# Kernel tuning notes

Hardware: AMD Instinct MI355X
Metric: run time of the kernel (lower is better)

The kernel has to match this reference:

```python
import jax, jax.numpy as jnp
import numpy as np

N_NODES = 50000
N_EDGES = 800000
D_FEAT = 64


def setup_inputs() -> dict:
    key = jax.random.key(0)
    k_h, k_src, k_dst = jax.random.split(key, 3)
    h = jax.random.normal(k_h, (N_NODES, D_FEAT), dtype=jnp.float32)
    src = jax.random.randint(k_src, (N_EDGES,), 0, N_NODES, dtype=jnp.int64)
    dst = jax.random.randint(k_dst, (N_EDGES,), 0, N_NODES, dtype=jnp.int64)
    return {"h": h, "src": src, "dst": dst}


def reference(h, src, dst):
    # DGL u_mul_v: per-edge elementwise product of source and destination node features.
    # z[e, :] = h[src[e], :] * h[dst[e], :]   -> shape [E, D]
    return h[src] * h[dst]
```

## Files before the change

kernel.cpp:

```cpp
#include <hip/hip_runtime.h>
#include <hip/hip_bf16.h>


#define D_FEAT 64
#define CHUNKS_PER_EDGE 16

__global__ __launch_bounds__(256) void hadamard_gather_kernel(
    const float* __restrict__ h,
    const int* __restrict__ src,
    const int* __restrict__ dst,
    float* __restrict__ out,
    int n_edges)
{
    int tid = blockIdx.x * blockDim.x + threadIdx.x;
    int e = tid >> 4;
    int c = tid & 15;
    if (e >= n_edges) return;

    long long s = src[e];
    long long d = dst[e];

    const float4* hs = reinterpret_cast<const float4*>(h + s * D_FEAT) + c;
    const float4* hd = reinterpret_cast<const float4*>(h + d * D_FEAT) + c;
    float4 a = *hs;
    float4 b = *hd;

    float4 r;
    r.x = a.x * b.x;
    r.y = a.y * b.y;
    r.z = a.z * b.z;
    r.w = a.w * b.w;

    reinterpret_cast<float4*>(out + (long long)e * D_FEAT)[c] = r;
}

extern "C" void kernel_launch(void* const* d_in, const int* in_sizes, int n_in,
                              void* d_out, int out_size, void* d_ws, size_t ws_size,
                              hipStream_t stream) {
    const float* h   = reinterpret_cast<const float*>(d_in[0]);
    const int*   src = reinterpret_cast<const int*>(d_in[1]);
    const int*   dst = reinterpret_cast<const int*>(d_in[2]);
    float* out = reinterpret_cast<float*>(d_out);

    int n_edges = in_sizes[1];
    int total_threads = n_edges * CHUNKS_PER_EDGE;
    int block = 256;
    int grid = (total_threads + block - 1) / block;

    hadamard_gather_kernel<<<grid, block, 0, stream>>>(h, src, dst, out, n_edges);
}
```

Before: 250.7 us.

## Use persistent grid-stride loop with batched gathers and nontemporal index loads/stores

Replaces the one-thread-chunk-per-edge launch with a fixed grid of 2000 blocks. Each 16-lane slot walks the edges in grid strides and processes them in batches of 5, loading all indices first, then all feature rows, then multiplying and storing. This raises memory-level parallelism per thread and cuts launch and scheduling overhead. Index loads and output stores use nontemporal hints so the streaming 205 MB output does not pollute cache. The risks are higher register use and a fixed grid size that may not suit every device.

```diff
diff --git a/kernel.cpp b/kernel.cpp
--- a/kernel.cpp
+++ b/kernel.cpp
@@ -3,35 +3,52 @@
 
 
 #define D_FEAT 64
-#define CHUNKS_PER_EDGE 16
+typedef float vf4 __attribute__((ext_vector_type(4)));
 
-__global__ __launch_bounds__(256) void hadamard_gather_kernel(
+constexpr int BLOCK = 256;
+constexpr int GRID  = 2000;
+constexpr int SLOTS = GRID * BLOCK / 16;
+constexpr int BATCH = 5;
+
+__global__ __launch_bounds__(BLOCK) void hadamard_gather_kernel(
     const float* __restrict__ h,
     const int* __restrict__ src,
     const int* __restrict__ dst,
     float* __restrict__ out,
     int n_edges)
 {
-    int tid = blockIdx.x * blockDim.x + threadIdx.x;
-    int e = tid >> 4;
-    int c = tid & 15;
-    if (e >= n_edges) return;
+    int tid  = blockIdx.x * BLOCK + threadIdx.x;
+    int slot = tid >> 4;
+    int c    = tid & 15;
 
-    long long s = src[e];
-    long long d = dst[e];
+    int iters = (n_edges - slot + SLOTS - 1) / SLOTS;
 
-    const float4* hs = reinterpret_cast<const float4*>(h + s * D_FEAT) + c;
-    const float4* hd = reinterpret_cast<const float4*>(h + d * D_FEAT) + c;
-    float4 a = *hs;
-    float4 b = *hd;
+    for (int it = 0; it < iters; it += BATCH) {
+        int nb = (iters - it) < BATCH ? (iters - it) : BATCH;
 
-    float4 r;
-    r.x = a.x * b.x;
-    r.y = a.y * b.y;
-    r.z = a.z * b.z;
-    r.w = a.w * b.w;
-
-    reinterpret_cast<float4*>(out + (long long)e * D_FEAT)[c] = r;
+        int e[BATCH], s[BATCH], d[BATCH];
+        for (int j = 0; j < BATCH; ++j) {
+            if (j < nb) {
+                e[j] = slot + (it + j) * SLOTS;
+                s[j] = __builtin_nontemporal_load(src + e[j]);
+                d[j] = __builtin_nontemporal_load(dst + e[j]);
+            }
+        }
+        vf4 a[BATCH], b[BATCH];
+        for (int j = 0; j < BATCH; ++j) {
+            if (j < nb) {
+                a[j] = reinterpret_cast<const vf4*>(h + (long long)s[j] * D_FEAT)[c];
+                b[j] = reinterpret_cast<const vf4*>(h + (long long)d[j] * D_FEAT)[c];
+            }
+        }
+        for (int j = 0; j < BATCH; ++j) {
+            if (j < nb) {
+                vf4 r = a[j] * b[j];
+                __builtin_nontemporal_store(
+                    r, reinterpret_cast<vf4*>(out + (long long)e[j] * D_FEAT) + c);
+            }
+        }
+    }
 }
 
 extern "C" void kernel_launch(void* const* d_in, const int* in_sizes, int n_in,
@@ -43,9 +60,6 @@
     float* out = reinterpret_cast<float*>(d_out);
 
     int n_edges = in_sizes[1];
-    int total_threads = n_edges * CHUNKS_PER_EDGE;
-    int block = 256;
-    int grid = (total_threads + block - 1) / block;
 
-    hadamard_gather_kernel<<<grid, block, 0, stream>>>(h, src, dst, out, n_edges);
+    hadamard_gather_kernel<<<GRID, BLOCK, 0, stream>>>(h, src, dst, out, n_edges);
 }
```

Measured after the change: 271.3 us. 8.2% more time.
